# Kernel tuning notes

Measured on AMD Instinct MI355X. Metric: run time of the kernel, lower is better.

## Reference

```python
import jax, jax.numpy as jnp
import numpy as np

N_NODES = 100000


def gcn_conv(x, edge_index, W, b, num_nodes):
    # PyG GCNConv default: add self-loops, symmetric normalization, bias.
    src = jnp.concatenate([edge_index[0], jnp.arange(num_nodes, dtype=edge_index.dtype)])
    dst = jnp.concatenate([edge_index[1], jnp.arange(num_nodes, dtype=edge_index.dtype)])
    # degree on the target side (flow source_to_target), edge weight = 1
    deg = jax.ops.segment_sum(jnp.ones_like(dst, dtype=x.dtype), dst, num_segments=num_nodes)
    dinv = jnp.where(deg > 0, jax.lax.rsqrt(deg), 0.0)
    norm = dinv[src] * dinv[dst]                      # [E+N]
    h = x @ W                                         # [N, out]
    msg = h[src] * norm[:, None]                      # [E+N, out]
    out = jax.ops.segment_sum(msg, dst, num_segments=num_nodes)  # [N, out]
    return out + b


def setup_inputs() -> dict:
    key = jax.random.key(0)
    k1, k2, k3, k4, k5, k6 = jax.random.split(key, 6)
    d_in, d_hid, d_out = 64, 64, 64
    x = jax.random.normal(k1, (N_NODES, d_in), dtype=jnp.float32)
    edge_index = jax.random.randint(k2, (2, 1000000), 0, N_NODES, dtype=jnp.int64)
    # Glorot-like init for weights, zero bias (as PyG GCNConv)
    W1 = jax.random.normal(k3, (d_in, d_hid), dtype=jnp.float32) / np.sqrt(d_in)
    b1 = jnp.zeros((d_hid,), dtype=jnp.float32)
    W2 = jax.random.normal(k4, (d_hid, d_out), dtype=jnp.float32) / np.sqrt(d_hid)
    b2 = jnp.zeros((d_out,), dtype=jnp.float32)
    return {"x": x, "edge_index": edge_index, "W1": W1, "b1": b1, "W2": W2, "b2": b2}


def reference(x, edge_index, W1, b1, W2, b2):
    n = x.shape[0]
    h = jax.nn.relu(gcn_conv(x, edge_index, W1, b1, n))
    out = jax.nn.relu(gcn_conv(h, edge_index, W2, b2, n))
    return out
```

## Files before the change

kernel.cpp:

```cpp
#include <hip/hip_runtime.h>

#define D 64
#define NB 256
#define BSHIFT 8

typedef unsigned int u32;
typedef unsigned short u16;
typedef short bf8v __attribute__((ext_vector_type(8)));
typedef float f4v __attribute__((ext_vector_type(4)));

__device__ __forceinline__ float bf_lo(u32 p) { return __uint_as_float(p << 16); }
__device__ __forceinline__ float bf_hi(u32 p) { return __uint_as_float(p & 0xffff0000u); }
__device__ __forceinline__ u32 bf_rne(float f) {
    u32 u = __float_as_uint(f);
    return (u + 0x7fffu + ((u >> 16) & 1u)) >> 16;
}

__global__ void cast_k(const float4* __restrict__ x, uint2* __restrict__ xb, int n4) {
    int i = blockIdx.x * blockDim.x + threadIdx.x;
    if (i < n4) {
        float4 v = x[i];
        uint2 o;
        o.x = bf_rne(v.x) | (bf_rne(v.y) << 16);
        o.y = bf_rne(v.z) | (bf_rne(v.w) << 16);
        xb[i] = o;
    }
}

__global__ __launch_bounds__(256) void hist_k(const int* __restrict__ dst,
                                              int* __restrict__ histT, int E, int chunk,
                                              int nbuck) {
    __shared__ int h[512];
    int t = threadIdx.x;
    for (int b = t; b < nbuck; b += 256) h[b] = 0;
    __syncthreads();
    int start = blockIdx.x * chunk;
    int endi = min(E, start + chunk);
    for (int j = start + t; j < endi; j += 256) atomicAdd(&h[dst[j] >> BSHIFT], 1);
    __syncthreads();
    for (int b = t; b < nbuck; b += 256) histT[b * NB + blockIdx.x] = h[b];
}

__global__ __launch_bounds__(1024) void gscan1_k(const int* __restrict__ in,
                                                 int* __restrict__ out,
                                                 int* __restrict__ partials, int M) {
    __shared__ int wsum[16];
    int t = threadIdx.x, wave = t >> 6, lane = t & 63;
    int i = blockIdx.x * 1024 + t;
    int v = (i < M) ? in[i] : 0;
    int x = v;
#pragma unroll
    for (int off = 1; off < 64; off <<= 1) {
        int y = __shfl_up(x, off, 64);
        if (lane >= off) x += y;
    }
    if (lane == 63) wsum[wave] = x;
    __syncthreads();
    if (wave == 0) {
        int s = (lane < 16) ? wsum[lane] : 0;
#pragma unroll
        for (int off = 1; off < 16; off <<= 1) {
            int y = __shfl_up(s, off, 64);
            if (lane >= off) s += y;
        }
        if (lane < 16) wsum[lane] = s;
    }
    __syncthreads();
    int woff = (wave > 0) ? wsum[wave - 1] : 0;
    if (i < M) out[i] = x + woff - v;
    if (t == 0) partials[blockIdx.x] = wsum[15];
}

__global__ __launch_bounds__(128) void scan2_k(const int* __restrict__ partials,
                                               int* __restrict__ blockoff,
                                               int* __restrict__ totalp, int nb) {
    __shared__ int s[128];
    int t = threadIdx.x;
    int v = (t < nb) ? partials[t] : 0;
    s[t] = v;
    __syncthreads();
    for (int off = 1; off < 128; off <<= 1) {
        int add = (t >= off) ? s[t - off] : 0;
        __syncthreads();
        s[t] += add;
        __syncthreads();
    }
    blockoff[t] = s[t] - v;
    if (t == nb - 1) *totalp = s[t];
}

__global__ void gadd_k(int* __restrict__ data, const int* __restrict__ blockoff, int M) {
    int i = blockIdx.x * blockDim.x + threadIdx.x;
    if (i < M) data[i] += blockoff[i >> 10];
}

__global__ __launch_bounds__(256) void bscat_k(const int* __restrict__ src,
                                               const int* __restrict__ dst,
                                               const int* __restrict__ segT,
                                               int2* __restrict__ pairs, int E, int chunk,
                                               int nbuck) {
    __shared__ int sbase[512];
    __shared__ int rank[512];
    int t = threadIdx.x;
    for (int b = t; b < nbuck; b += 256) {
        sbase[b] = segT[b * NB + blockIdx.x];
        rank[b] = 0;
    }
    __syncthreads();
    int start = blockIdx.x * chunk;
    int endi = min(E, start + chunk);
    for (int j = start + t; j < endi; j += 256) {
        int d = dst[j];
        int b = d >> BSHIFT;
        int pos = sbase[b] + atomicAdd(&rank[b], 1);
        pairs[pos] = make_int2(src[j], d);
    }
}

__global__ __launch_bounds__(256) void bcount_k(const int2* __restrict__ pairs,
                                                const int* __restrict__ segT,
                                                int* __restrict__ cnt, int N, int nbuck,
                                                int E) {
    __shared__ int c[1 << BSHIFT];
    int t = threadIdx.x;
    int b = blockIdx.x;
    int base = b << BSHIFT;
    c[t] = 0;
    __syncthreads();
    int s0 = segT[b * NB];
    int s1 = (b + 1 < nbuck) ? segT[(b + 1) * NB] : E;
    for (int j = s0 + t; j < s1; j += 256) atomicAdd(&c[pairs[j].y - base], 1);
    __syncthreads();
    int n = base + t;
    if (n < N) cnt[n] = c[t];
}

__global__ __launch_bounds__(1024) void scan1_k(const int* __restrict__ cnt,
                                                int* __restrict__ row,
                                                int* __restrict__ partials, int N) {
    __shared__ int wsum[16];
    int t = threadIdx.x, wave = t >> 6, lane = t & 63;
    int i = blockIdx.x * 1024 + t;
    int v = (i < N) ? ((cnt[i] + 16) & ~15) : 0;
    int x = v;
#pragma unroll
    for (int off = 1; off < 64; off <<= 1) {
        int y = __shfl_up(x, off, 64);
        if (lane >= off) x += y;
    }
    if (lane == 63) wsum[wave] = x;
    __syncthreads();
    if (wave == 0) {
        int s = (lane < 16) ? wsum[lane] : 0;
#pragma unroll
        for (int off = 1; off < 16; off <<= 1) {
            int y = __shfl_up(s, off, 64);
            if (lane >= off) s += y;
        }
        if (lane < 16) wsum[lane] = s;
    }
    __syncthreads();
    int woff = (wave > 0) ? wsum[wave - 1] : 0;
    if (i < N) row[i] = x + woff - v;
    if (t == 0) partials[blockIdx.x] = wsum[15];
}

__global__ void scan3_k(int* __restrict__ row, const int* __restrict__ blockoff,
                        const int* __restrict__ cnt, float* __restrict__ dinv, int N) {
    int i = blockIdx.x * blockDim.x + threadIdx.x;
    if (i < N) {
        row[i] += blockoff[i >> 10];
        dinv[i] = rsqrtf((float)cnt[i] + 1.0f);
    }
}

__global__ __launch_bounds__(256) void bfill_k(const int2* __restrict__ pairs,
                                               const int* __restrict__ segT,
                                               const int* __restrict__ row,
                                               const float* __restrict__ dinv,
                                               int2* __restrict__ pr, int N, int nbuck,
                                               int E) {
    __shared__ int cur[1 << BSHIFT];
    int t = threadIdx.x;
    int b = blockIdx.x;
    int base = b << BSHIFT;
    int n = base + t;
    if (n < N) {
        int r = row[n];
        float di = dinv[n];
        pr[r] = make_int2(n, __float_as_int(di * di));
        cur[t] = r + 1;
    }
    __syncthreads();
    int s0 = segT[b * NB];
    int s1 = (b + 1 < nbuck) ? segT[(b + 1) * NB] : E;
    for (int j = s0 + t; j < s1; j += 256) {
        int2 e = pairs[j];
        int pos = atomicAdd(&cur[e.y - base], 1);
        pr[pos] = make_int2(e.x, __float_as_int(dinv[e.x] * dinv[e.y]));
    }
    __syncthreads();
    if (n < N) {
        int e = row[n + 1];
        for (int pos = cur[t]; pos < e; ++pos) pr[pos] = make_int2(n, 0);
    }
}

__global__ __launch_bounds__(256) void gemm_k(const u32* __restrict__ hb,
                                              const float* __restrict__ W,
                                              u16* __restrict__ hout, int N) {
    int t = threadIdx.x;
    int lane = t & 63;
    int m = lane & 15;
    int quad = lane >> 4;
    bf8v Bf[2][4];
#pragma unroll
    for (int kc = 0; kc < 2; ++kc)
#pragma unroll
        for (int nb = 0; nb < 4; ++nb)
#pragma unroll
            for (int j = 0; j < 8; ++j)
                Bf[kc][nb][j] = (short)bf_rne(W[(32 * kc + 8 * quad + j) * D + m + 16 * nb]);
    int ngroups = (N + 15) >> 4;
    int g = blockIdx.x * 4 + (t >> 6);
    int stride = gridDim.x * 4;
    for (; g < ngroups; g += stride) {
        int base = g * 16;
        int r0 = base + m;
        if (r0 >= N) r0 = N - 1;
        f4v acc[4] = {{0.f, 0.f, 0.f, 0.f},
                      {0.f, 0.f, 0.f, 0.f},
                      {0.f, 0.f, 0.f, 0.f},
                      {0.f, 0.f, 0.f, 0.f}};
#pragma unroll
        for (int kc = 0; kc < 2; ++kc) {
            bf8v Af = *(const bf8v*)(hb + (size_t)r0 * 32 + kc * 16 + quad * 4);
#pragma unroll
            for (int nb = 0; nb < 4; ++nb)
                acc[nb] = __builtin_amdgcn_mfma_f32_16x16x32_bf16(Af, Bf[kc][nb], acc[nb],
                                                                  0, 0, 0);
        }
#pragma unroll
        for (int nb = 0; nb < 4; ++nb)
#pragma unroll
            for (int r = 0; r < 4; ++r) {
                int rowi = base + quad * 4 + r;
                if (rowi < N)
                    hout[(size_t)rowi * D + nb * 16 + m] = (u16)bf_rne(acc[nb][r]);
            }
    }
}

__global__ __launch_bounds__(256) void agg_k(const uint2* __restrict__ inb2,
                                             const int* __restrict__ row,
                                             const int2* __restrict__ pr,
                                             const float* __restrict__ b,
                                             float* __restrict__ out_f32,
                                             u16* __restrict__ out_b16, int N) {
    int t = threadIdx.x;
    int lane = t & 63;
    int p = lane & 15;
    int q = lane >> 4;
    float4 bias = *(const float4*)(b + 4 * p);
    int wid = blockIdx.x * 4 + (t >> 6);
    int nw = gridDim.x * 4;
    for (int i = wid; i < N; i += nw) {
        int beg = row[i], end = row[i + 1];
        float v0 = 0.f, v1 = 0.f, v2 = 0.f, v3 = 0.f;
        for (int j = beg; j < end; j += 16) {
            int2 e0 = pr[j + q];
            int2 e1 = pr[j + 4 + q];
            int2 e2 = pr[j + 8 + q];
            int2 e3 = pr[j + 12 + q];
            uint2 g0 = inb2[(size_t)e0.x * 16 + p];
            uint2 g1 = inb2[(size_t)e1.x * 16 + p];
            uint2 g2 = inb2[(size_t)e2.x * 16 + p];
            uint2 g3 = inb2[(size_t)e3.x * 16 + p];
            float w0 = __int_as_float(e0.y);
            float w1 = __int_as_float(e1.y);
            float w2 = __int_as_float(e2.y);
            float w3 = __int_as_float(e3.y);
            v0 = fmaf(bf_lo(g0.x), w0, v0);
            v1 = fmaf(bf_hi(g0.x), w0, v1);
            v2 = fmaf(bf_lo(g0.y), w0, v2);
            v3 = fmaf(bf_hi(g0.y), w0, v3);
            v0 = fmaf(bf_lo(g1.x), w1, v0);
            v1 = fmaf(bf_hi(g1.x), w1, v1);
            v2 = fmaf(bf_lo(g1.y), w1, v2);
            v3 = fmaf(bf_hi(g1.y), w1, v3);
            v0 = fmaf(bf_lo(g2.x), w2, v0);
            v1 = fmaf(bf_hi(g2.x), w2, v1);
            v2 = fmaf(bf_lo(g2.y), w2, v2);
            v3 = fmaf(bf_hi(g2.y), w2, v3);
            v0 = fmaf(bf_lo(g3.x), w3, v0);
            v1 = fmaf(bf_hi(g3.x), w3, v1);
            v2 = fmaf(bf_lo(g3.y), w3, v2);
            v3 = fmaf(bf_hi(g3.y), w3, v3);
        }
        v0 += __shfl_xor(v0, 16, 64);
        v1 += __shfl_xor(v1, 16, 64);
        v2 += __shfl_xor(v2, 16, 64);
        v3 += __shfl_xor(v3, 16, 64);
        v0 += __shfl_xor(v0, 32, 64);
        v1 += __shfl_xor(v1, 32, 64);
        v2 += __shfl_xor(v2, 32, 64);
        v3 += __shfl_xor(v3, 32, 64);
        v0 = fmaxf(v0 + bias.x, 0.f);
        v1 = fmaxf(v1 + bias.y, 0.f);
        v2 = fmaxf(v2 + bias.z, 0.f);
        v3 = fmaxf(v3 + bias.w, 0.f);
        if (q == 0) {
            if (out_b16) {
                uint2 o;
                o.x = bf_rne(v0) | (bf_rne(v1) << 16);
                o.y = bf_rne(v2) | (bf_rne(v3) << 16);
                *(uint2*)(out_b16 + (size_t)i * D + 4 * p) = o;
            } else {
                *(float4*)(out_f32 + (size_t)i * D + 4 * p) =
                    make_float4(v0, v1, v2, v3);
            }
        }
    }
}


extern "C" void kernel_launch(void* const* d_in, const int* in_sizes, int n_in,
                              void* d_out, int out_size, void* d_ws, size_t ws_size,
                              hipStream_t stream) {
    const float* x  = (const float*)d_in[0];
    const int*   ei = (const int*)d_in[1];
    const float* W1 = (const float*)d_in[2];
    const float* b1 = (const float*)d_in[3];
    const float* W2 = (const float*)d_in[4];
    const float* b2 = (const float*)d_in[5];
    float* out = (float*)d_out;

    int N = in_sizes[0] / D;
    int E = in_sizes[1] / 2;
    const int* src = ei;
    const int* dst = ei + E;

    int nbuck = (N + (1 << BSHIFT) - 1) >> BSHIFT;
    int chunk = (E + NB - 1) / NB;
    int M = nbuck * NB;
    int Emax = E + 16 * N + 64;

    char* ws = (char*)d_ws;
    size_t off = 0;
    auto align256 = [](size_t v) { return (v + 255) & ~(size_t)255; };
    int* cnt = (int*)(ws + off);       off += align256((size_t)N * 4);
    int* row = (int*)(ws + off);       off += align256((size_t)(N + 1) * 4);
    float* dinv = (float*)(ws + off);  off += align256((size_t)N * 4);
    int* partials = (int*)(ws + off);  off += 512;
    int* blockoff = (int*)(ws + off);  off += 512;
    int* partials2 = (int*)(ws + off); off += 512;
    int* blockoff2 = (int*)(ws + off); off += 512;
    int* scratch = (int*)(ws + off);   off += 256;
    int* histT = (int*)(ws + off);     off += align256((size_t)M * 4);
    int2* pairs = (int2*)(ws + off);   off += align256((size_t)E * 8);
    int2* pr = (int2*)(ws + off);      off += align256((size_t)Emax * 8);
    u32* xb = (u32*)(ws + off);        off += align256((size_t)N * D * 2);
    u16* h = (u16*)(ws + off);         off += align256((size_t)N * D * 2);
    u16* buf16 = (u16*)(ws + off);     off += align256((size_t)N * D * 2);

    dim3 b256(256);
    int nb = (N + 1023) / 1024;
    int nbG = (M + 1023) / 1024;

    cast_k<<<(N * D / 4 + 255) / 256, b256, 0, stream>>>((const float4*)x, (uint2*)xb,
                                                         N * D / 4);
    hist_k<<<NB, b256, 0, stream>>>(dst, histT, E, chunk, nbuck);
    gscan1_k<<<nbG, 1024, 0, stream>>>(histT, histT, partials2, M);
    scan2_k<<<1, 128, 0, stream>>>(partials2, blockoff2, scratch, nbG);
    gadd_k<<<(M + 255) / 256, b256, 0, stream>>>(histT, blockoff2, M);
    bscat_k<<<NB, b256, 0, stream>>>(src, dst, histT, pairs, E, chunk, nbuck);
    bcount_k<<<nbuck, b256, 0, stream>>>(pairs, histT, cnt, N, nbuck, E);
    scan1_k<<<nb, 1024, 0, stream>>>(cnt, row, partials, N);
    scan2_k<<<1, 128, 0, stream>>>(partials, blockoff, row + N, nb);
    scan3_k<<<(N + 255) / 256, b256, 0, stream>>>(row, blockoff, cnt, dinv, N);
    bfill_k<<<nbuck, b256, 0, stream>>>(pairs, histT, row, dinv, pr, N, nbuck, E);

    int ngroups = (N + 15) / 16;
    int gemm_blocks = (ngroups + 3) / 4;

    gemm_k<<<gemm_blocks, b256, 0, stream>>>(xb, W1, h, N);
    agg_k<<<2560, b256, 0, stream>>>((const uint2*)h, row, pr, b1, nullptr, buf16, N);
    gemm_k<<<gemm_blocks, b256, 0, stream>>>((const u32*)buf16, W2, h, N);
    agg_k<<<2560, b256, 0, stream>>>((const uint2*)h, row, pr, b2, out, nullptr, N);
}
```

Baseline: 233.7 us.

## Replace CSR scan with fixed 32-slot per-node blocks plus linked overflow chains

The exclusive scan over padded degrees (scan1/scan2/scan3) is removed. Each node now gets a fixed 32-slot block in the edge list, and overflow blocks are allocated with a global atomic counter and chained through a flag slot. Aggregation walks these chains with 8-lane groups that each load 16 bytes (8 bf16 features), using 128-bit loads for both edges and features. This cuts three launches and the row array, but pads every node to at least 32 slots: much more memory traffic, since average degree is about 10, plus extra padding work in bfill and the agg loop.

```diff
diff --git a/kernel.cpp b/kernel.cpp
--- a/kernel.cpp
+++ b/kernel.cpp
@@ -3,6 +3,8 @@
 #define D 64
 #define NB 256
 #define BSHIFT 8
+#define SLOTS 32
+#define MAXCONT 65536
 
 typedef unsigned int u32;
 typedef unsigned short u16;
@@ -16,8 +18,10 @@
     return (u + 0x7fffu + ((u >> 16) & 1u)) >> 16;
 }
 
-__global__ void cast_k(const float4* __restrict__ x, uint2* __restrict__ xb, int n4) {
+__global__ void cast_k(const float4* __restrict__ x, uint2* __restrict__ xb, int n4,
+                       int* __restrict__ ovf) {
     int i = blockIdx.x * blockDim.x + threadIdx.x;
+    if (i == 0) *ovf = 0;
     if (i < n4) {
         float4 v = x[i];
         uint2 o;
@@ -119,7 +123,8 @@
 
 __global__ __launch_bounds__(256) void bcount_k(const int2* __restrict__ pairs,
                                                 const int* __restrict__ segT,
-                                                int* __restrict__ cnt, int N, int nbuck,
+                                                int* __restrict__ cnt,
+                                                float* __restrict__ dinv, int N, int nbuck,
                                                 int E) {
     __shared__ int c[1 << BSHIFT];
     int t = threadIdx.x;
@@ -132,77 +137,73 @@
     for (int j = s0 + t; j < s1; j += 256) atomicAdd(&c[pairs[j].y - base], 1);
     __syncthreads();
     int n = base + t;
-    if (n < N) cnt[n] = c[t];
-}
-
-__global__ __launch_bounds__(1024) void scan1_k(const int* __restrict__ cnt,
-                                                int* __restrict__ row,
-                                                int* __restrict__ partials, int N) {
-    __shared__ int wsum[16];
-    int t = threadIdx.x, wave = t >> 6, lane = t & 63;
-    int i = blockIdx.x * 1024 + t;
-    int v = (i < N) ? ((cnt[i] + 16) & ~15) : 0;
-    int x = v;
-#pragma unroll
-    for (int off = 1; off < 64; off <<= 1) {
-        int y = __shfl_up(x, off, 64);
-        if (lane >= off) x += y;
-    }
-    if (lane == 63) wsum[wave] = x;
-    __syncthreads();
-    if (wave == 0) {
-        int s = (lane < 16) ? wsum[lane] : 0;
-#pragma unroll
-        for (int off = 1; off < 16; off <<= 1) {
-            int y = __shfl_up(s, off, 64);
-            if (lane >= off) s += y;
-        }
-        if (lane < 16) wsum[lane] = s;
-    }
-    __syncthreads();
-    int woff = (wave > 0) ? wsum[wave - 1] : 0;
-    if (i < N) row[i] = x + woff - v;
-    if (t == 0) partials[blockIdx.x] = wsum[15];
-}
-
-__global__ void scan3_k(int* __restrict__ row, const int* __restrict__ blockoff,
-                        const int* __restrict__ cnt, float* __restrict__ dinv, int N) {
-    int i = blockIdx.x * blockDim.x + threadIdx.x;
-    if (i < N) {
-        row[i] += blockoff[i >> 10];
-        dinv[i] = rsqrtf((float)cnt[i] + 1.0f);
+    if (n < N) {
+        cnt[n] = c[t];
+        dinv[n] = rsqrtf((float)c[t] + 1.0f);
     }
 }
 
 __global__ __launch_bounds__(256) void bfill_k(const int2* __restrict__ pairs,
                                                const int* __restrict__ segT,
-                                               const int* __restrict__ row,
+                                               const int* __restrict__ cnt,
                                                const float* __restrict__ dinv,
-                                               int2* __restrict__ pr, int N, int nbuck,
-                                               int E) {
+                                               int2* __restrict__ pr, int* __restrict__ ovf,
+                                               int N, int nbuck, int E) {
     __shared__ int cur[1 << BSHIFT];
+    __shared__ int cbase[1 << BSHIFT];
     int t = threadIdx.x;
     int b = blockIdx.x;
     int base = b << BSHIFT;
     int n = base + t;
+    int nblk = 0;
     if (n < N) {
-        int r = row[n];
+        int c = cnt[n];
         float di = dinv[n];
-        pr[r] = make_int2(n, __float_as_int(di * di));
-        cur[t] = r + 1;
+        pr[(size_t)n * SLOTS] = make_int2(n, __float_as_int(di * di));
+        nblk = (c > 30) ? (c / 31) : 0;
+        int cb = 0;
+        if (nblk) cb = atomicAdd(ovf, nblk);
+        cbase[t] = cb;
+        cur[t] = 1;
+        if (nblk == 0) {
+            pr[(size_t)n * SLOTS + 31] = make_int2(n, 0);
+        } else {
+            pr[(size_t)n * SLOTS + 31] = make_int2(cb, (int)0x80000000u);
+            for (int k = 0; k < nblk; ++k) {
+                size_t cs = (size_t)N * SLOTS + (size_t)(cb + k) * SLOTS + 31;
+                pr[cs] = (k < nblk - 1) ? make_int2(cb + k + 1, (int)0x80000000u)
+                                        : make_int2(n, 0);
+            }
+        }
     }
     __syncthreads();
     int s0 = segT[b * NB];
     int s1 = (b + 1 < nbuck) ? segT[(b + 1) * NB] : E;
     for (int j = s0 + t; j < s1; j += 256) {
         int2 e = pairs[j];
-        int pos = atomicAdd(&cur[e.y - base], 1);
-        pr[pos] = make_int2(e.x, __float_as_int(dinv[e.x] * dinv[e.y]));
+        int local = e.y - base;
+        int pos = atomicAdd(&cur[local], 1);
+        size_t phys;
+        if (pos < 31)
+            phys = (size_t)e.y * SLOTS + pos;
+        else
+            phys = (size_t)N * SLOTS +
+                   (size_t)(cbase[local] + (pos - 31) / 31) * SLOTS + (pos - 31) % 31;
+        pr[phys] = make_int2(e.x, __float_as_int(dinv[e.x] * dinv[e.y]));
     }
     __syncthreads();
     if (n < N) {
-        int e = row[n + 1];
-        for (int pos = cur[t]; pos < e; ++pos) pr[pos] = make_int2(n, 0);
+        int total = 31 + 31 * nblk;
+        int cb = cbase[t];
+        for (int pos = cur[t]; pos < total; ++pos) {
+            size_t phys;
+            if (pos < 31)
+                phys = (size_t)n * SLOTS + pos;
+            else
+                phys = (size_t)N * SLOTS + (size_t)(cb + (pos - 31) / 31) * SLOTS +
+                       (pos - 31) % 31;
+            pr[phys] = make_int2(n, 0);
+        }
     }
 }
 
@@ -251,73 +252,84 @@
     }
 }
 
-__global__ __launch_bounds__(256) void agg_k(const uint2* __restrict__ inb2,
-                                             const int* __restrict__ row,
+__global__ __launch_bounds__(256) void agg_k(const uint4* __restrict__ h4,
                                              const int2* __restrict__ pr,
                                              const float* __restrict__ b,
                                              float* __restrict__ out_f32,
                                              u16* __restrict__ out_b16, int N) {
     int t = threadIdx.x;
     int lane = t & 63;
-    int p = lane & 15;
-    int q = lane >> 4;
-    float4 bias = *(const float4*)(b + 4 * p);
+    int p = lane & 7;
+    int q = lane >> 3;
+    float4 ba = *(const float4*)(b + 8 * p);
+    float4 bb = *(const float4*)(b + 8 * p + 4);
     int wid = blockIdx.x * 4 + (t >> 6);
     int nw = gridDim.x * 4;
     for (int i = wid; i < N; i += nw) {
-        int beg = row[i], end = row[i + 1];
         float v0 = 0.f, v1 = 0.f, v2 = 0.f, v3 = 0.f;
-        for (int j = beg; j < end; j += 16) {
-            int2 e0 = pr[j + q];
-            int2 e1 = pr[j + 4 + q];
-            int2 e2 = pr[j + 8 + q];
-            int2 e3 = pr[j + 12 + q];
-            uint2 g0 = inb2[(size_t)e0.x * 16 + p];
-            uint2 g1 = inb2[(size_t)e1.x * 16 + p];
-            uint2 g2 = inb2[(size_t)e2.x * 16 + p];
-            uint2 g3 = inb2[(size_t)e3.x * 16 + p];
-            float w0 = __int_as_float(e0.y);
-            float w1 = __int_as_float(e1.y);
-            float w2 = __int_as_float(e2.y);
-            float w3 = __int_as_float(e3.y);
-            v0 = fmaf(bf_lo(g0.x), w0, v0);
-            v1 = fmaf(bf_hi(g0.x), w0, v1);
-            v2 = fmaf(bf_lo(g0.y), w0, v2);
-            v3 = fmaf(bf_hi(g0.y), w0, v3);
-            v0 = fmaf(bf_lo(g1.x), w1, v0);
-            v1 = fmaf(bf_hi(g1.x), w1, v1);
-            v2 = fmaf(bf_lo(g1.y), w1, v2);
-            v3 = fmaf(bf_hi(g1.y), w1, v3);
-            v0 = fmaf(bf_lo(g2.x), w2, v0);
-            v1 = fmaf(bf_hi(g2.x), w2, v1);
-            v2 = fmaf(bf_lo(g2.y), w2, v2);
-            v3 = fmaf(bf_hi(g2.y), w2, v3);
-            v0 = fmaf(bf_lo(g3.x), w3, v0);
-            v1 = fmaf(bf_hi(g3.x), w3, v1);
-            v2 = fmaf(bf_lo(g3.y), w3, v2);
-            v3 = fmaf(bf_hi(g3.y), w3, v3);
-        }
-        v0 += __shfl_xor(v0, 16, 64);
-        v1 += __shfl_xor(v1, 16, 64);
-        v2 += __shfl_xor(v2, 16, 64);
-        v3 += __shfl_xor(v3, 16, 64);
-        v0 += __shfl_xor(v0, 32, 64);
-        v1 += __shfl_xor(v1, 32, 64);
-        v2 += __shfl_xor(v2, 32, 64);
-        v3 += __shfl_xor(v3, 32, 64);
-        v0 = fmaxf(v0 + bias.x, 0.f);
-        v1 = fmaxf(v1 + bias.y, 0.f);
-        v2 = fmaxf(v2 + bias.z, 0.f);
-        v3 = fmaxf(v3 + bias.w, 0.f);
+        float v4 = 0.f, v5 = 0.f, v6 = 0.f, v7 = 0.f;
+        int4 el1;
+        const int2* bp = pr + (size_t)i * SLOTS;
+        for (;;) {
+            int4 el0 = ((const int4*)bp)[q];
+            el1 = ((const int4*)bp)[8 + q];
+            uint4 g0 = h4[(size_t)(u32)el0.x * 8 + p];
+            uint4 g1 = h4[(size_t)(u32)el0.z * 8 + p];
+            uint4 g2 = h4[(size_t)(u32)el1.x * 8 + p];
+            uint4 g3 = h4[(size_t)(u32)el1.z * 8 + p];
+            float w0 = __int_as_float(el0.y);
+            float w1 = __int_as_float(el0.w);
+            float w2 = __int_as_float(el1.y);
+            float w3 = __int_as_float(el1.w);
+            v0 = fmaf(bf_lo(g0.x), w0, v0); v1 = fmaf(bf_hi(g0.x), w0, v1);
+            v2 = fmaf(bf_lo(g0.y), w0, v2); v3 = fmaf(bf_hi(g0.y), w0, v3);
+            v4 = fmaf(bf_lo(g0.z), w0, v4); v5 = fmaf(bf_hi(g0.z), w0, v5);
+            v6 = fmaf(bf_lo(g0.w), w0, v6); v7 = fmaf(bf_hi(g0.w), w0, v7);
+            v0 = fmaf(bf_lo(g1.x), w1, v0); v1 = fmaf(bf_hi(g1.x), w1, v1);
+            v2 = fmaf(bf_lo(g1.y), w1, v2); v3 = fmaf(bf_hi(g1.y), w1, v3);
+            v4 = fmaf(bf_lo(g1.z), w1, v4); v5 = fmaf(bf_hi(g1.z), w1, v5);
+            v6 = fmaf(bf_lo(g1.w), w1, v6); v7 = fmaf(bf_hi(g1.w), w1, v7);
+            v0 = fmaf(bf_lo(g2.x), w2, v0); v1 = fmaf(bf_hi(g2.x), w2, v1);
+            v2 = fmaf(bf_lo(g2.y), w2, v2); v3 = fmaf(bf_hi(g2.y), w2, v3);
+            v4 = fmaf(bf_lo(g2.z), w2, v4); v5 = fmaf(bf_hi(g2.z), w2, v5);
+            v6 = fmaf(bf_lo(g2.w), w2, v6); v7 = fmaf(bf_hi(g2.w), w2, v7);
+            v0 = fmaf(bf_lo(g3.x), w3, v0); v1 = fmaf(bf_hi(g3.x), w3, v1);
+            v2 = fmaf(bf_lo(g3.y), w3, v2); v3 = fmaf(bf_hi(g3.y), w3, v3);
+            v4 = fmaf(bf_lo(g3.z), w3, v4); v5 = fmaf(bf_hi(g3.z), w3, v5);
+            v6 = fmaf(bf_lo(g3.w), w3, v6); v7 = fmaf(bf_hi(g3.w), w3, v7);
+            int flag = __shfl(el1.w, 63, 64);
+            if (flag >= 0) break;
+            int c = __shfl(el1.z, 63, 64);
+            bp = pr + (size_t)N * SLOTS + (size_t)c * SLOTS;
+        }
+        v0 += __shfl_xor(v0, 8, 64);  v1 += __shfl_xor(v1, 8, 64);
+        v2 += __shfl_xor(v2, 8, 64);  v3 += __shfl_xor(v3, 8, 64);
+        v4 += __shfl_xor(v4, 8, 64);  v5 += __shfl_xor(v5, 8, 64);
+        v6 += __shfl_xor(v6, 8, 64);  v7 += __shfl_xor(v7, 8, 64);
+        v0 += __shfl_xor(v0, 16, 64); v1 += __shfl_xor(v1, 16, 64);
+        v2 += __shfl_xor(v2, 16, 64); v3 += __shfl_xor(v3, 16, 64);
+        v4 += __shfl_xor(v4, 16, 64); v5 += __shfl_xor(v5, 16, 64);
+        v6 += __shfl_xor(v6, 16, 64); v7 += __shfl_xor(v7, 16, 64);
+        v0 += __shfl_xor(v0, 32, 64); v1 += __shfl_xor(v1, 32, 64);
+        v2 += __shfl_xor(v2, 32, 64); v3 += __shfl_xor(v3, 32, 64);
+        v4 += __shfl_xor(v4, 32, 64); v5 += __shfl_xor(v5, 32, 64);
+        v6 += __shfl_xor(v6, 32, 64); v7 += __shfl_xor(v7, 32, 64);
+        v0 = fmaxf(v0 + ba.x, 0.f); v1 = fmaxf(v1 + ba.y, 0.f);
+        v2 = fmaxf(v2 + ba.z, 0.f); v3 = fmaxf(v3 + ba.w, 0.f);
+        v4 = fmaxf(v4 + bb.x, 0.f); v5 = fmaxf(v5 + bb.y, 0.f);
+        v6 = fmaxf(v6 + bb.z, 0.f); v7 = fmaxf(v7 + bb.w, 0.f);
         if (q == 0) {
             if (out_b16) {
-                uint2 o;
+                uint4 o;
                 o.x = bf_rne(v0) | (bf_rne(v1) << 16);
                 o.y = bf_rne(v2) | (bf_rne(v3) << 16);
-                *(uint2*)(out_b16 + (size_t)i * D + 4 * p) = o;
+                o.z = bf_rne(v4) | (bf_rne(v5) << 16);
+                o.w = bf_rne(v6) | (bf_rne(v7) << 16);
+                *(uint4*)(out_b16 + (size_t)i * D + 8 * p) = o;
             } else {
-                *(float4*)(out_f32 + (size_t)i * D + 4 * p) =
-                    make_float4(v0, v1, v2, v3);
+                float* dst = out_f32 + (size_t)i * D + 8 * p;
+                *(float4*)dst = make_float4(v0, v1, v2, v3);
+                *(float4*)(dst + 4) = make_float4(v4, v5, v6, v7);
             }
         }
     }
@@ -343,48 +355,41 @@
     int nbuck = (N + (1 << BSHIFT) - 1) >> BSHIFT;
     int chunk = (E + NB - 1) / NB;
     int M = nbuck * NB;
-    int Emax = E + 16 * N + 64;
 
     char* ws = (char*)d_ws;
     size_t off = 0;
     auto align256 = [](size_t v) { return (v + 255) & ~(size_t)255; };
     int* cnt = (int*)(ws + off);       off += align256((size_t)N * 4);
-    int* row = (int*)(ws + off);       off += align256((size_t)(N + 1) * 4);
     float* dinv = (float*)(ws + off);  off += align256((size_t)N * 4);
-    int* partials = (int*)(ws + off);  off += 512;
-    int* blockoff = (int*)(ws + off);  off += 512;
     int* partials2 = (int*)(ws + off); off += 512;
     int* blockoff2 = (int*)(ws + off); off += 512;
     int* scratch = (int*)(ws + off);   off += 256;
+    int* ovf = (int*)(ws + off);       off += 256;
     int* histT = (int*)(ws + off);     off += align256((size_t)M * 4);
     int2* pairs = (int2*)(ws + off);   off += align256((size_t)E * 8);
-    int2* pr = (int2*)(ws + off);      off += align256((size_t)Emax * 8);
+    int2* pr = (int2*)(ws + off);      off += align256(((size_t)N + MAXCONT) * SLOTS * 8);
     u32* xb = (u32*)(ws + off);        off += align256((size_t)N * D * 2);
     u16* h = (u16*)(ws + off);         off += align256((size_t)N * D * 2);
     u16* buf16 = (u16*)(ws + off);     off += align256((size_t)N * D * 2);
 
     dim3 b256(256);
-    int nb = (N + 1023) / 1024;
     int nbG = (M + 1023) / 1024;
 
     cast_k<<<(N * D / 4 + 255) / 256, b256, 0, stream>>>((const float4*)x, (uint2*)xb,
-                                                         N * D / 4);
+                                                         N * D / 4, ovf);
     hist_k<<<NB, b256, 0, stream>>>(dst, histT, E, chunk, nbuck);
     gscan1_k<<<nbG, 1024, 0, stream>>>(histT, histT, partials2, M);
     scan2_k<<<1, 128, 0, stream>>>(partials2, blockoff2, scratch, nbG);
     gadd_k<<<(M + 255) / 256, b256, 0, stream>>>(histT, blockoff2, M);
     bscat_k<<<NB, b256, 0, stream>>>(src, dst, histT, pairs, E, chunk, nbuck);
-    bcount_k<<<nbuck, b256, 0, stream>>>(pairs, histT, cnt, N, nbuck, E);
-    scan1_k<<<nb, 1024, 0, stream>>>(cnt, row, partials, N);
-    scan2_k<<<1, 128, 0, stream>>>(partials, blockoff, row + N, nb);
-    scan3_k<<<(N + 255) / 256, b256, 0, stream>>>(row, blockoff, cnt, dinv, N);
-    bfill_k<<<nbuck, b256, 0, stream>>>(pairs, histT, row, dinv, pr, N, nbuck, E);
+    bcount_k<<<nbuck, b256, 0, stream>>>(pairs, histT, cnt, dinv, N, nbuck, E);
+    bfill_k<<<nbuck, b256, 0, stream>>>(pairs, histT, cnt, dinv, pr, ovf, N, nbuck, E);
 
     int ngroups = (N + 15) / 16;
     int gemm_blocks = (ngroups + 3) / 4;
 
     gemm_k<<<gemm_blocks, b256, 0, stream>>>(xb, W1, h, N);
-    agg_k<<<2560, b256, 0, stream>>>((const uint2*)h, row, pr, b1, nullptr, buf16, N);
+    agg_k<<<2560, b256, 0, stream>>>((const uint4*)h, pr, b1, nullptr, buf16, N);
     gemm_k<<<gemm_blocks, b256, 0, stream>>>((const u32*)buf16, W2, h, N);
-    agg_k<<<2560, b256, 0, stream>>>((const uint2*)h, row, pr, b2, out, nullptr, N);
-}
+    agg_k<<<2560, b256, 0, stream>>>((const uint4*)h, pr, b2, out, nullptr, N);
+}
```

Measured after the change: 227.3 us. -2.7%, faster.
